# Optimization experiments

Measured on AMD Instinct MI355X. Metric: run time of the kernel, lower is better.

## Reference

```python
import jax, jax.numpy as jnp
import numpy as np

B, T, C, HS = 4, 2048, 1024, 64  # batch, seq, n_embd, head_size


def setup_inputs() -> dict:
    key = jax.random.key(0)
    k1, k2, k3, k4 = jax.random.split(key, 4)
    x = jax.random.normal(k1, (B, T, C), dtype=jnp.float32)
    Wq = jax.random.normal(k2, (HS, C), dtype=jnp.float32) * (C ** -0.5)
    Wk = jax.random.normal(k3, (HS, C), dtype=jnp.float32) * (C ** -0.5)
    Wv = jax.random.normal(k4, (HS, C), dtype=jnp.float32) * (C ** -0.5)
    return {"x": x, "Wq": Wq, "Wk": Wk, "Wv": Wv}


def reference(x, Wq, Wk, Wv):
    # q,k,v: [B,T,HS] (nn.Linear: x @ W.T, no bias)
    q = jnp.einsum('btc,hc->bth', x, Wq)
    k = jnp.einsum('btc,hc->bth', x, Wk)
    v = jnp.einsum('btc,hc->bth', x, Wv)
    scale = k.shape[-1] ** -0.5
    wei = jnp.einsum('bth,bsh->bts', q, k) * scale  # [B,T,T]
    # causal mask (tril == 0 -> -inf)
    mask = jnp.tril(jnp.ones((T, T), dtype=bool))
    wei = jnp.where(mask, wei, -jnp.inf)
    wei = jax.nn.softmax(wei, axis=-1)
    # dropout p=0.0 -> identity
    out = jnp.einsum('bts,bsh->bth', wei, v)  # [B,T,HS]
    return out
```

## Files before the change

kernel.cpp:

```cpp
#include <hip/hip_runtime.h>
#include <hip/hip_bf16.h>

#define BB 4
#define TT 2048
#define CC 1024
#define HSZ 64
#define NTOT 8192

typedef __attribute__((ext_vector_type(8))) short bf16x8;
typedef __attribute__((ext_vector_type(4))) float f32x4;

__device__ __forceinline__ unsigned short f2bf(float x) {
    __hip_bfloat16 h = __float2bfloat16(x);
    return *reinterpret_cast<unsigned short*>(&h);
}

__global__ __launch_bounds__(256) void convert_w(
    const float* __restrict__ Wq, const float* __restrict__ Wk,
    const float* __restrict__ Wv, unsigned short* __restrict__ Wh) {
    const int i = blockIdx.x * 256 + threadIdx.x;
    const int c = i >> 8, k4 = (i & 255) * 4;
    float4 wv;
    if (c < 64) {
        wv = *(const float4*)&Wq[(size_t)c * CC + k4];
        wv.x *= 0.125f; wv.y *= 0.125f; wv.z *= 0.125f; wv.w *= 0.125f;
    } else if (c < 128) {
        wv = *(const float4*)&Wk[(size_t)(c - 64) * CC + k4];
    } else {
        wv = *(const float4*)&Wv[(size_t)(c - 128) * CC + k4];
    }
    ushort4 h = {f2bf(wv.x), f2bf(wv.y), f2bf(wv.z), f2bf(wv.w)};
    *(ushort4*)&Wh[(size_t)c * CC + k4] = h;
}

__global__ __launch_bounds__(256, 2) void qkv_mfma(
    const float* __restrict__ x, const unsigned short* __restrict__ Wh,
    unsigned short* __restrict__ qs, unsigned short* __restrict__ ksb,
    unsigned short* __restrict__ vT) {
    __shared__ __align__(16) unsigned short xs[16 * 1032];
    __shared__ __align__(16) unsigned short Ws[192 * 72];
    const int tid = threadIdx.x;
    const int w = tid >> 6, lane = tid & 63;
    const int l16 = lane & 15, quad = lane >> 4;
    const int row0 = blockIdx.x * 16;

#pragma unroll
    for (int it = 0; it < 16; ++it) {
        float4 xv = *(const float4*)&x[(size_t)(row0 + it) * CC + tid * 4];
        ushort4 h = {f2bf(xv.x), f2bf(xv.y), f2bf(xv.z), f2bf(xv.w)};
        *(ushort4*)&xs[it * 1032 + tid * 4] = h;
    }

    f32x4 acc[3];
#pragma unroll
    for (int i = 0; i < 3; ++i) acc[i] = (f32x4){0.f, 0.f, 0.f, 0.f};

    for (int ch = 0; ch < 16; ++ch) {
#pragma unroll
        for (int it = 0; it < 6; ++it) {
            const int e = tid + it * 256;
            const int c = e >> 3, g = e & 7;
            *(uint4*)&Ws[c * 72 + g * 8] =
                *(const uint4*)&Wh[(size_t)c * CC + ch * 64 + g * 8];
        }
        __syncthreads();
        bf16x8 a0 = *(const bf16x8*)&xs[l16 * 1032 + ch * 64 + quad * 8];
        bf16x8 a1 = *(const bf16x8*)&xs[l16 * 1032 + ch * 64 + 32 + quad * 8];
#pragma unroll
        for (int i = 0; i < 3; ++i) {
            const int t = w * 3 + i;
            bf16x8 b0 = *(const bf16x8*)&Ws[(t * 16 + l16) * 72 + quad * 8];
            bf16x8 b1 = *(const bf16x8*)&Ws[(t * 16 + l16) * 72 + 32 + quad * 8];
            f32x4 a = acc[i];
            a = __builtin_amdgcn_mfma_f32_16x16x32_bf16(a0, b0, a, 0, 0, 0);
            a = __builtin_amdgcn_mfma_f32_16x16x32_bf16(a1, b1, a, 0, 0, 0);
            acc[i] = a;
        }
        __syncthreads();
    }

#pragma unroll
    for (int i = 0; i < 3; ++i) {
        const int t = w * 3 + i;
        const int col = t * 16 + l16;
        f32x4 a = acc[i];
        if (t < 4) {
#pragma unroll
            for (int r = 0; r < 4; ++r)
                qs[(size_t)(row0 + quad * 4 + r) * HSZ + col] = f2bf(a[r]);
        } else if (t < 8) {
#pragma unroll
            for (int r = 0; r < 4; ++r)
                ksb[(size_t)(row0 + quad * 4 + r) * HSZ + (col - 64)] = f2bf(a[r]);
        } else {
            ushort4 pk = {f2bf(a[0]), f2bf(a[1]), f2bf(a[2]), f2bf(a[3])};
            *(ushort4*)&vT[(size_t)(col - 128) * NTOT + row0 + quad * 4] = pk;
        }
    }
}

__global__ __launch_bounds__(256, 2) void attn_mfma(
    const unsigned short* __restrict__ qs, const unsigned short* __restrict__ ksb,
    const unsigned short* __restrict__ vT, float* __restrict__ out) {
    __shared__ __align__(16) unsigned char smem[17664];
    unsigned short* Ps = (unsigned short*)smem;
    float* Om = (float*)smem;
    float* Lm = (float*)(smem + 17408);

    const int raw = blockIdx.x;
    const int i = (raw < 256) ? raw : 767 - raw;
    const int b = i >> 7;
    const int qt = i & 127;
    const int t0 = qt * 16;
    const int tid = threadIdx.x;
    const int w = tid >> 6, lane = tid & 63;
    const int l16 = lane & 15, quad = lane >> 4;

    const size_t qoff = (size_t)(b * TT + t0 + l16) * HSZ + quad * 8;
    const bf16x8 aq0 = *(const bf16x8*)&qs[qoff];
    const bf16x8 aq1 = *(const bf16x8*)&qs[qoff + 32];

    f32x4 OC[4];
#pragma unroll
    for (int t = 0; t < 4; ++t) OC[t] = (f32x4){0.f, 0.f, 0.f, 0.f};
    float lsum[4] = {0.f, 0.f, 0.f, 0.f};

    const unsigned short* kbase = ksb + (size_t)b * TT * HSZ;
    const int nk = (qt >> 2) + 1;

    for (int j = w; j < nk; j += 4) {
        const int key0 = j * 64;
        bf16x8 cv0[4], cv1[4];
#pragma unroll
        for (int ht = 0; ht < 4; ++ht) {
            const unsigned short* vp =
                vT + (size_t)(ht * 16 + l16) * NTOT + b * TT + key0 + quad * 8;
            cv0[ht] = *(const bf16x8*)vp;
            cv1[ht] = *(const bf16x8*)(vp + 32);
        }
        f32x4 S[4];
#pragma unroll
        for (int nt = 0; nt < 4; ++nt) {
            const unsigned short* kp =
                kbase + (size_t)(key0 + nt * 16 + l16) * HSZ + quad * 8;
            bf16x8 bk0 = *(const bf16x8*)kp;
            bf16x8 bk1 = *(const bf16x8*)(kp + 32);
            f32x4 a = (f32x4){0.f, 0.f, 0.f, 0.f};
            __builtin_amdgcn_s_setprio(1);
            a = __builtin_amdgcn_mfma_f32_16x16x32_bf16(aq0, bk0, a, 0, 0, 0);
            a = __builtin_amdgcn_mfma_f32_16x16x32_bf16(aq1, bk1, a, 0, 0, 0);
            __builtin_amdgcn_s_setprio(0);
            S[nt] = a;
        }
        if (j == nk - 1) {
#pragma unroll
            for (int nt = 0; nt < 4; ++nt) {
                const int key = key0 + nt * 16 + l16;
#pragma unroll
                for (int r = 0; r < 4; ++r)
                    if (key > t0 + quad * 4 + r) S[nt][r] = -1e30f;
            }
        }
#pragma unroll
        for (int nt = 0; nt < 4; ++nt)
#pragma unroll
            for (int r = 0; r < 4; ++r) S[nt][r] = __expf(S[nt][r]);
#pragma unroll
        for (int r = 0; r < 4; ++r)
            lsum[r] += S[0][r] + S[1][r] + S[2][r] + S[3][r];
        unsigned short* Pw = Ps + w * 1152;
#pragma unroll
        for (int nt = 0; nt < 4; ++nt)
#pragma unroll
            for (int r = 0; r < 4; ++r)
                Pw[(quad * 4 + r) * 72 + nt * 16 + l16] = f2bf(S[nt][r]);
        bf16x8 pf0 = *(const bf16x8*)&Pw[l16 * 72 + quad * 8];
        bf16x8 pf1 = *(const bf16x8*)&Pw[l16 * 72 + 32 + quad * 8];
        __builtin_amdgcn_s_setprio(1);
#pragma unroll
        for (int ht = 0; ht < 4; ++ht) {
            f32x4 a = OC[ht];
            a = __builtin_amdgcn_mfma_f32_16x16x32_bf16(pf0, cv0[ht], a, 0, 0, 0);
            a = __builtin_amdgcn_mfma_f32_16x16x32_bf16(pf1, cv1[ht], a, 0, 0, 0);
            OC[ht] = a;
        }
        __builtin_amdgcn_s_setprio(0);
    }
#pragma unroll
    for (int r = 0; r < 4; ++r) {
        float v = lsum[r];
#pragma unroll
        for (int off = 1; off < 16; off <<= 1) v += __shfl_xor(v, off, 64);
        lsum[r] = v;
    }
    __syncthreads();
#pragma unroll
    for (int ht = 0; ht < 4; ++ht)
#pragma unroll
        for (int r = 0; r < 4; ++r)
            Om[(w * 16 + quad * 4 + r) * 68 + ht * 16 + l16] = OC[ht][r];
    if (l16 == 0) {
#pragma unroll
        for (int r = 0; r < 4; ++r) Lm[w * 16 + quad * 4 + r] = lsum[r];
    }
    __syncthreads();
    {
        const int row = tid >> 4, h0 = (tid & 15) * 4;
        float L = 0.f, o0 = 0.f, o1 = 0.f, o2 = 0.f, o3 = 0.f;
#pragma unroll
        for (int w2 = 0; w2 < 4; ++w2) {
            L += Lm[w2 * 16 + row];
            const float* p = &Om[(w2 * 16 + row) * 68 + h0];
            o0 += p[0]; o1 += p[1]; o2 += p[2]; o3 += p[3];
        }
        const float inv = 1.f / L;
        *(float4*)&out[(size_t)(b * TT + t0 + row) * HSZ + h0] =
            (float4){o0 * inv, o1 * inv, o2 * inv, o3 * inv};
    }
}

extern "C" void kernel_launch(void* const* d_in, const int* in_sizes, int n_in,
                              void* d_out, int out_size, void* d_ws, size_t ws_size,
                              hipStream_t stream) {
    const float* x  = (const float*)d_in[0];
    const float* Wq = (const float*)d_in[1];
    const float* Wk = (const float*)d_in[2];
    const float* Wv = (const float*)d_in[3];
    float* out = (float*)d_out;

    unsigned short* qs = (unsigned short*)d_ws;
    unsigned short* ksb = qs + (size_t)NTOT * HSZ;
    unsigned short* vT = ksb + (size_t)NTOT * HSZ;
    unsigned short* Wh = vT + (size_t)NTOT * HSZ;

    convert_w<<<192, 256, 0, stream>>>(Wq, Wk, Wv, Wh);
    qkv_mfma<<<512, 256, 0, stream>>>(x, Wh, qs, ksb, vT);
    attn_mfma<<<512, 256, 0, stream>>>(qs, ksb, vT, out);
}
```

Measured before the change: 114.3 us.

## Double-buffer QKV projection via registers with 32-row tiles and drop setprio

The QKV projection kernel now handles 32 rows per block instead of 16, so each weight chunk staged in LDS feeds twice as many MFMAs and the grid shrinks to 256 blocks. It also stops staging all of x upfront: each 64-column chunk of x and W is prefetched into registers for the next iteration while the current chunk is computed, then written to LDS between barriers. This is meant to cut weight reloads and hide global load latency. In exchange, 256 blocks may underfill the CUs, and register pressure goes up. The attention kernel also drops its s_setprio hints.

Result: faster. 108.6 us (-5.0%).

```diff
diff --git a/kernel.cpp b/kernel.cpp
--- a/kernel.cpp
+++ b/kernel.cpp
@@ -33,70 +33,122 @@
     *(ushort4*)&Wh[(size_t)c * CC + k4] = h;
 }
 
-__global__ __launch_bounds__(256, 2) void qkv_mfma(
+__global__ __launch_bounds__(256) void qkv_mfma(
     const float* __restrict__ x, const unsigned short* __restrict__ Wh,
     unsigned short* __restrict__ qs, unsigned short* __restrict__ ksb,
     unsigned short* __restrict__ vT) {
-    __shared__ __align__(16) unsigned short xs[16 * 1032];
+    __shared__ __align__(16) unsigned short xs[32 * 72];
     __shared__ __align__(16) unsigned short Ws[192 * 72];
     const int tid = threadIdx.x;
     const int w = tid >> 6, lane = tid & 63;
     const int l16 = lane & 15, quad = lane >> 4;
-    const int row0 = blockIdx.x * 16;
-
-#pragma unroll
-    for (int it = 0; it < 16; ++it) {
-        float4 xv = *(const float4*)&x[(size_t)(row0 + it) * CC + tid * 4];
-        ushort4 h = {f2bf(xv.x), f2bf(xv.y), f2bf(xv.z), f2bf(xv.w)};
-        *(ushort4*)&xs[it * 1032 + tid * 4] = h;
-    }
-
-    f32x4 acc[3];
-#pragma unroll
-    for (int i = 0; i < 3; ++i) acc[i] = (f32x4){0.f, 0.f, 0.f, 0.f};
+    const int row0 = blockIdx.x * 32;
+
+    const int xrow = tid >> 3, xcol = (tid & 7) * 8;
+
+    float4 xa, xb;
+    uint4 wreg0, wreg1, wreg2, wreg3, wreg4, wreg5;
+
+#define LOADX(ch)                                                            \
+    {                                                                        \
+        const float* p = &x[(size_t)(row0 + xrow) * CC + (ch) * 64 + xcol];  \
+        xa = *(const float4*)p;                                              \
+        xb = *(const float4*)(p + 4);                                        \
+    }
+#define LOADW1(it, dst, ch)                                                  \
+    {                                                                        \
+        const int e = tid + (it) * 256;                                      \
+        const int c = e >> 3, g = e & 7;                                     \
+        dst = *(const uint4*)&Wh[(size_t)c * CC + (ch) * 64 + g * 8];        \
+    }
+#define LOADW(ch)                                                            \
+    LOADW1(0, wreg0, ch) LOADW1(1, wreg1, ch) LOADW1(2, wreg2, ch)           \
+    LOADW1(3, wreg3, ch) LOADW1(4, wreg4, ch) LOADW1(5, wreg5, ch)
+#define STOREW1(it, src)                                                     \
+    {                                                                        \
+        const int e = tid + (it) * 256;                                      \
+        const int c = e >> 3, g = e & 7;                                     \
+        *(uint4*)&Ws[c * 72 + g * 8] = src;                                  \
+    }
+#define WRITELDS()                                                           \
+    {                                                                        \
+        ushort4 h0 = {f2bf(xa.x), f2bf(xa.y), f2bf(xa.z), f2bf(xa.w)};       \
+        ushort4 h1 = {f2bf(xb.x), f2bf(xb.y), f2bf(xb.z), f2bf(xb.w)};       \
+        *(ushort4*)&xs[xrow * 72 + xcol] = h0;                               \
+        *(ushort4*)&xs[xrow * 72 + xcol + 4] = h1;                           \
+        STOREW1(0, wreg0) STOREW1(1, wreg1) STOREW1(2, wreg2)                \
+        STOREW1(3, wreg3) STOREW1(4, wreg4) STOREW1(5, wreg5)                \
+    }
+
+    f32x4 acc[2][3];
+#pragma unroll
+    for (int m = 0; m < 2; ++m)
+#pragma unroll
+        for (int n = 0; n < 3; ++n) acc[m][n] = (f32x4){0.f, 0.f, 0.f, 0.f};
+
+    LOADX(0);
+    LOADW(0);
+    WRITELDS();
+    __syncthreads();
 
     for (int ch = 0; ch < 16; ++ch) {
-#pragma unroll
-        for (int it = 0; it < 6; ++it) {
-            const int e = tid + it * 256;
-            const int c = e >> 3, g = e & 7;
-            *(uint4*)&Ws[c * 72 + g * 8] =
-                *(const uint4*)&Wh[(size_t)c * CC + ch * 64 + g * 8];
-        }
-        __syncthreads();
-        bf16x8 a0 = *(const bf16x8*)&xs[l16 * 1032 + ch * 64 + quad * 8];
-        bf16x8 a1 = *(const bf16x8*)&xs[l16 * 1032 + ch * 64 + 32 + quad * 8];
-#pragma unroll
-        for (int i = 0; i < 3; ++i) {
-            const int t = w * 3 + i;
-            bf16x8 b0 = *(const bf16x8*)&Ws[(t * 16 + l16) * 72 + quad * 8];
-            bf16x8 b1 = *(const bf16x8*)&Ws[(t * 16 + l16) * 72 + 32 + quad * 8];
-            f32x4 a = acc[i];
-            a = __builtin_amdgcn_mfma_f32_16x16x32_bf16(a0, b0, a, 0, 0, 0);
-            a = __builtin_amdgcn_mfma_f32_16x16x32_bf16(a1, b1, a, 0, 0, 0);
-            acc[i] = a;
-        }
-        __syncthreads();
-    }
-
-#pragma unroll
-    for (int i = 0; i < 3; ++i) {
-        const int t = w * 3 + i;
-        const int col = t * 16 + l16;
-        f32x4 a = acc[i];
-        if (t < 4) {
-#pragma unroll
-            for (int r = 0; r < 4; ++r)
-                qs[(size_t)(row0 + quad * 4 + r) * HSZ + col] = f2bf(a[r]);
-        } else if (t < 8) {
-#pragma unroll
-            for (int r = 0; r < 4; ++r)
-                ksb[(size_t)(row0 + quad * 4 + r) * HSZ + (col - 64)] = f2bf(a[r]);
-        } else {
-            ushort4 pk = {f2bf(a[0]), f2bf(a[1]), f2bf(a[2]), f2bf(a[3])};
-            *(ushort4*)&vT[(size_t)(col - 128) * NTOT + row0 + quad * 4] = pk;
-        }
-    }
+        if (ch < 15) {
+            LOADX(ch + 1);
+            LOADW(ch + 1);
+        }
+        bf16x8 am[2][2], bn[3][2];
+#pragma unroll
+        for (int m = 0; m < 2; ++m)
+#pragma unroll
+            for (int h = 0; h < 2; ++h)
+                am[m][h] = *(const bf16x8*)&xs[(m * 16 + l16) * 72 + h * 32 + quad * 8];
+#pragma unroll
+        for (int n = 0; n < 3; ++n)
+#pragma unroll
+            for (int h = 0; h < 2; ++h)
+                bn[n][h] =
+                    *(const bf16x8*)&Ws[(w * 48 + n * 16 + l16) * 72 + h * 32 + quad * 8];
+#pragma unroll
+        for (int h = 0; h < 2; ++h)
+#pragma unroll
+            for (int m = 0; m < 2; ++m)
+#pragma unroll
+                for (int n = 0; n < 3; ++n)
+                    acc[m][n] = __builtin_amdgcn_mfma_f32_16x16x32_bf16(
+                        am[m][h], bn[n][h], acc[m][n], 0, 0, 0);
+        if (ch < 15) {
+            __syncthreads();
+            WRITELDS();
+            __syncthreads();
+        }
+    }
+
+#pragma unroll
+    for (int m = 0; m < 2; ++m) {
+#pragma unroll
+        for (int n = 0; n < 3; ++n) {
+            const int col = w * 48 + n * 16 + l16;
+            const int r0 = row0 + m * 16 + quad * 4;
+            f32x4 a = acc[m][n];
+            if (col < 64) {
+#pragma unroll
+                for (int r = 0; r < 4; ++r)
+                    qs[(size_t)(r0 + r) * HSZ + col] = f2bf(a[r]);
+            } else if (col < 128) {
+#pragma unroll
+                for (int r = 0; r < 4; ++r)
+                    ksb[(size_t)(r0 + r) * HSZ + (col - 64)] = f2bf(a[r]);
+            } else {
+                ushort4 pk = {f2bf(a[0]), f2bf(a[1]), f2bf(a[2]), f2bf(a[3])};
+                *(ushort4*)&vT[(size_t)(col - 128) * NTOT + r0] = pk;
+            }
+        }
+    }
+#undef LOADX
+#undef LOADW1
+#undef LOADW
+#undef STOREW1
+#undef WRITELDS
 }
 
 __global__ __launch_bounds__(256, 2) void attn_mfma(
@@ -146,10 +198,8 @@
             bf16x8 bk0 = *(const bf16x8*)kp;
             bf16x8 bk1 = *(const bf16x8*)(kp + 32);
             f32x4 a = (f32x4){0.f, 0.f, 0.f, 0.f};
-            __builtin_amdgcn_s_setprio(1);
             a = __builtin_amdgcn_mfma_f32_16x16x32_bf16(aq0, bk0, a, 0, 0, 0);
             a = __builtin_amdgcn_mfma_f32_16x16x32_bf16(aq1, bk1, a, 0, 0, 0);
-            __builtin_amdgcn_s_setprio(0);
             S[nt] = a;
         }
         if (j == nk - 1) {
@@ -176,7 +226,6 @@
                 Pw[(quad * 4 + r) * 72 + nt * 16 + l16] = f2bf(S[nt][r]);
         bf16x8 pf0 = *(const bf16x8*)&Pw[l16 * 72 + quad * 8];
         bf16x8 pf1 = *(const bf16x8*)&Pw[l16 * 72 + 32 + quad * 8];
-        __builtin_amdgcn_s_setprio(1);
 #pragma unroll
         for (int ht = 0; ht < 4; ++ht) {
             f32x4 a = OC[ht];
@@ -184,7 +233,6 @@
             a = __builtin_amdgcn_mfma_f32_16x16x32_bf16(pf1, cv1[ht], a, 0, 0, 0);
             OC[ht] = a;
         }
-        __builtin_amdgcn_s_setprio(0);
     }
 #pragma unroll
     for (int r = 0; r < 4; ++r) {
@@ -234,6 +282,6 @@
     unsigned short* Wh = vT + (size_t)NTOT * HSZ;
 
     convert_w<<<192, 256, 0, stream>>>(Wq, Wk, Wv, Wh);
-    qkv_mfma<<<512, 256, 0, stream>>>(x, Wh, qs, ksb, vT);
+    qkv_mfma<<<256, 256, 0, stream>>>(x, Wh, qs, ksb, vT);
     attn_mfma<<<512, 256, 0, stream>>>(qs, ksb, vT, out);
 }
```

## Double-buffer QKV projection with larger 32-row tiles and drop setprio in attention

Applied to the files above, without the earlier changes.

The QKV projection kernel now processes 32 rows per block with 512 threads arranged as a 2x4 warp grid. It streams x and W in 64-wide K chunks through double-buffered LDS, prefetching the next chunk into registers while the current one is computed. This replaces the full-row x staging and the two barriers per chunk, aiming to hide global load latency and halve the W traffic per output row. The attention kernel also drops its s_setprio hints around the MFMA blocks, which may change how waves are scheduled against each other.

After: 110.6 us. -3.2%, faster.

```diff
diff --git a/kernel.cpp b/kernel.cpp
--- a/kernel.cpp
+++ b/kernel.cpp
@@ -33,70 +33,99 @@
     *(ushort4*)&Wh[(size_t)c * CC + k4] = h;
 }
 
-__global__ __launch_bounds__(256, 2) void qkv_mfma(
+__global__ __launch_bounds__(512) void qkv_mfma(
     const float* __restrict__ x, const unsigned short* __restrict__ Wh,
     unsigned short* __restrict__ qs, unsigned short* __restrict__ ksb,
     unsigned short* __restrict__ vT) {
-    __shared__ __align__(16) unsigned short xs[16 * 1032];
-    __shared__ __align__(16) unsigned short Ws[192 * 72];
+    __shared__ __align__(16) unsigned short xs[2][32 * 72];
+    __shared__ __align__(16) unsigned short Ws[2][192 * 72];
     const int tid = threadIdx.x;
     const int w = tid >> 6, lane = tid & 63;
     const int l16 = lane & 15, quad = lane >> 4;
-    const int row0 = blockIdx.x * 16;
-
-#pragma unroll
-    for (int it = 0; it < 16; ++it) {
-        float4 xv = *(const float4*)&x[(size_t)(row0 + it) * CC + tid * 4];
-        ushort4 h = {f2bf(xv.x), f2bf(xv.y), f2bf(xv.z), f2bf(xv.w)};
-        *(ushort4*)&xs[it * 1032 + tid * 4] = h;
+    const int wm = w >> 2, wn = w & 3;
+    const int row0 = blockIdx.x * 32;
+
+    const int xrow = tid >> 4, xcol = (tid & 15) * 4;
+    const int c0 = (tid + 0) >> 3, g0 = (tid + 0) & 7;
+    const int c1 = (tid + 512) >> 3, g1 = (tid + 512) & 7;
+    const int c2 = (tid + 1024) >> 3, g2 = (tid + 1024) & 7;
+
+    float4 xa;
+    uint4 w0, w1, w2;
+
+#define LOADX(ch) \
+    xa = *(const float4*)&x[(size_t)(row0 + xrow) * CC + (ch) * 64 + xcol];
+#define LOADW(ch)                                                      \
+    w0 = *(const uint4*)&Wh[(size_t)c0 * CC + (ch) * 64 + g0 * 8];     \
+    w1 = *(const uint4*)&Wh[(size_t)c1 * CC + (ch) * 64 + g1 * 8];     \
+    w2 = *(const uint4*)&Wh[(size_t)c2 * CC + (ch) * 64 + g2 * 8];
+#define WRITELDS(buf)                                                  \
+    {                                                                  \
+        ushort4 h = {f2bf(xa.x), f2bf(xa.y), f2bf(xa.z), f2bf(xa.w)}; \
+        *(ushort4*)&xs[buf][xrow * 72 + xcol] = h;                     \
+        *(uint4*)&Ws[buf][c0 * 72 + g0 * 8] = w0;                      \
+        *(uint4*)&Ws[buf][c1 * 72 + g1 * 8] = w1;                      \
+        *(uint4*)&Ws[buf][c2 * 72 + g2 * 8] = w2;                      \
     }
 
     f32x4 acc[3];
 #pragma unroll
-    for (int i = 0; i < 3; ++i) acc[i] = (f32x4){0.f, 0.f, 0.f, 0.f};
+    for (int n = 0; n < 3; ++n) acc[n] = (f32x4){0.f, 0.f, 0.f, 0.f};
+
+    LOADX(0);
+    LOADW(0);
+    WRITELDS(0);
+    __syncthreads();
 
     for (int ch = 0; ch < 16; ++ch) {
-#pragma unroll
-        for (int it = 0; it < 6; ++it) {
-            const int e = tid + it * 256;
-            const int c = e >> 3, g = e & 7;
-            *(uint4*)&Ws[c * 72 + g * 8] =
-                *(const uint4*)&Wh[(size_t)c * CC + ch * 64 + g * 8];
-        }
-        __syncthreads();
-        bf16x8 a0 = *(const bf16x8*)&xs[l16 * 1032 + ch * 64 + quad * 8];
-        bf16x8 a1 = *(const bf16x8*)&xs[l16 * 1032 + ch * 64 + 32 + quad * 8];
-#pragma unroll
-        for (int i = 0; i < 3; ++i) {
-            const int t = w * 3 + i;
-            bf16x8 b0 = *(const bf16x8*)&Ws[(t * 16 + l16) * 72 + quad * 8];
-            bf16x8 b1 = *(const bf16x8*)&Ws[(t * 16 + l16) * 72 + 32 + quad * 8];
-            f32x4 a = acc[i];
-            a = __builtin_amdgcn_mfma_f32_16x16x32_bf16(a0, b0, a, 0, 0, 0);
-            a = __builtin_amdgcn_mfma_f32_16x16x32_bf16(a1, b1, a, 0, 0, 0);
-            acc[i] = a;
-        }
-        __syncthreads();
-    }
-
-#pragma unroll
-    for (int i = 0; i < 3; ++i) {
-        const int t = w * 3 + i;
-        const int col = t * 16 + l16;
-        f32x4 a = acc[i];
-        if (t < 4) {
+        if (ch < 15) {
+            LOADX(ch + 1);
+            LOADW(ch + 1);
+        }
+        const int cur = ch & 1;
+        bf16x8 am[2], bn[3][2];
+#pragma unroll
+        for (int h = 0; h < 2; ++h)
+            am[h] = *(const bf16x8*)&xs[cur][(wm * 16 + l16) * 72 + h * 32 + quad * 8];
+#pragma unroll
+        for (int n = 0; n < 3; ++n)
+#pragma unroll
+            for (int h = 0; h < 2; ++h)
+                bn[n][h] = *(const bf16x8*)&Ws[cur][(wn * 48 + n * 16 + l16) * 72 +
+                                                    h * 32 + quad * 8];
+#pragma unroll
+        for (int h = 0; h < 2; ++h)
+#pragma unroll
+            for (int n = 0; n < 3; ++n)
+                acc[n] = __builtin_amdgcn_mfma_f32_16x16x32_bf16(am[h], bn[n][h],
+                                                                 acc[n], 0, 0, 0);
+        if (ch < 15) {
+            WRITELDS(cur ^ 1);
+            __syncthreads();
+        }
+    }
+
+#pragma unroll
+    for (int n = 0; n < 3; ++n) {
+        const int col = wn * 48 + n * 16 + l16;
+        const int r0 = row0 + wm * 16 + quad * 4;
+        f32x4 a = acc[n];
+        if (col < 64) {
 #pragma unroll
             for (int r = 0; r < 4; ++r)
-                qs[(size_t)(row0 + quad * 4 + r) * HSZ + col] = f2bf(a[r]);
-        } else if (t < 8) {
+                qs[(size_t)(r0 + r) * HSZ + col] = f2bf(a[r]);
+        } else if (col < 128) {
 #pragma unroll
             for (int r = 0; r < 4; ++r)
-                ksb[(size_t)(row0 + quad * 4 + r) * HSZ + (col - 64)] = f2bf(a[r]);
+                ksb[(size_t)(r0 + r) * HSZ + (col - 64)] = f2bf(a[r]);
         } else {
             ushort4 pk = {f2bf(a[0]), f2bf(a[1]), f2bf(a[2]), f2bf(a[3])};
-            *(ushort4*)&vT[(size_t)(col - 128) * NTOT + row0 + quad * 4] = pk;
-        }
-    }
+            *(ushort4*)&vT[(size_t)(col - 128) * NTOT + r0] = pk;
+        }
+    }
+#undef LOADX
+#undef LOADW
+#undef WRITELDS
 }
 
 __global__ __launch_bounds__(256, 2) void attn_mfma(
@@ -146,10 +175,8 @@
             bf16x8 bk0 = *(const bf16x8*)kp;
             bf16x8 bk1 = *(const bf16x8*)(kp + 32);
             f32x4 a = (f32x4){0.f, 0.f, 0.f, 0.f};
-            __builtin_amdgcn_s_setprio(1);
             a = __builtin_amdgcn_mfma_f32_16x16x32_bf16(aq0, bk0, a, 0, 0, 0);
             a = __builtin_amdgcn_mfma_f32_16x16x32_bf16(aq1, bk1, a, 0, 0, 0);
-            __builtin_amdgcn_s_setprio(0);
             S[nt] = a;
         }
         if (j == nk - 1) {
@@ -176,7 +203,6 @@
                 Pw[(quad * 4 + r) * 72 + nt * 16 + l16] = f2bf(S[nt][r]);
         bf16x8 pf0 = *(const bf16x8*)&Pw[l16 * 72 + quad * 8];
         bf16x8 pf1 = *(const bf16x8*)&Pw[l16 * 72 + 32 + quad * 8];
-        __builtin_amdgcn_s_setprio(1);
 #pragma unroll
         for (int ht = 0; ht < 4; ++ht) {
             f32x4 a = OC[ht];
@@ -184,7 +210,6 @@
             a = __builtin_amdgcn_mfma_f32_16x16x32_bf16(pf1, cv1[ht], a, 0, 0, 0);
             OC[ht] = a;
         }
-        __builtin_amdgcn_s_setprio(0);
     }
 #pragma unroll
     for (int r = 0; r < 4; ++r) {
@@ -234,6 +259,6 @@
     unsigned short* Wh = vT + (size_t)NTOT * HSZ;
 
     convert_w<<<192, 256, 0, stream>>>(Wq, Wk, Wv, Wh);
-    qkv_mfma<<<512, 256, 0, stream>>>(x, Wh, qs, ksb, vT);
+    qkv_mfma<<<256, 512, 0, stream>>>(x, Wh, qs, ksb, vT);
     attn_mfma<<<512, 256, 0, stream>>>(qs, ksb, vT, out);
 }
```
